# Kernel tuning notes

Measured on AMD Instinct MI355X. Metric: run time of the kernel, lower is better.

## Reference

```python
import jax, jax.numpy as jnp
import numpy as np

N_HEADS = 32
N_KV_HEADS = 8
HEAD_DIM = 64


def _apply_rope(x, cos, sin):
    # x: [b, s, h, d]; cos/sin: [s, d//2]; interleaved real/imag pairs
    xr = x[..., 0::2]
    xi = x[..., 1::2]
    c = cos[None, :, None, :]
    s = sin[None, :, None, :]
    out_r = xr * c - xi * s
    out_i = xr * s + xi * c
    return jnp.stack([out_r, out_i], axis=-1).reshape(x.shape)


def setup_inputs() -> dict:
    key = jax.random.key(0)
    ks = jax.random.split(key, 10)
    b, s, dim = 2, 512, 2048
    cache_len = 1536
    half = HEAD_DIM // 2
    pos = jnp.arange(cache_len, cache_len + s, dtype=jnp.float32)
    inv_freq = 1.0 / (10000.0 ** (jnp.arange(0, half, dtype=jnp.float32) / half))
    ang = pos[:, None] * inv_freq[None, :]
    scale = 0.02
    return {
        "x": jax.random.normal(ks[0], (b, s, dim), jnp.float32),
        "freqs_cos": jnp.cos(ang),
        "freqs_sin": jnp.sin(ang),
        "k_cache": jax.random.normal(ks[1], (b, N_KV_HEADS, cache_len, HEAD_DIM), jnp.float32),
        "v_cache": jax.random.normal(ks[2], (b, N_KV_HEADS, cache_len, HEAD_DIM), jnp.float32),
        "attn_mask": jnp.zeros((s, cache_len + s), jnp.float32),
        "wq": jax.random.normal(ks[3], (N_HEADS * HEAD_DIM, dim), jnp.float32) * scale,
        "wk": jax.random.normal(ks[4], (N_KV_HEADS * HEAD_DIM, dim), jnp.float32) * scale,
        "wv": jax.random.normal(ks[5], (N_KV_HEADS * HEAD_DIM, dim), jnp.float32) * scale,
        "wo": jax.random.normal(ks[6], (dim, N_HEADS * HEAD_DIM), jnp.float32) * scale,
    }


def reference(x, freqs_cos, freqs_sin, k_cache, v_cache, attn_mask, wq, wk, wv, wo):
    b, s, dim = x.shape
    n_rep = N_HEADS // N_KV_HEADS
    # QKV projections (nn.Linear: y = x @ W.T)
    q = (x @ wq.T).reshape(b, s, N_HEADS, HEAD_DIM)
    k = (x @ wk.T).reshape(b, s, N_KV_HEADS, HEAD_DIM)
    v = (x @ wv.T).reshape(b, s, N_KV_HEADS, HEAD_DIM)
    # RoPE on q, k
    q = _apply_rope(q, freqs_cos, freqs_sin)
    k = _apply_rope(k, freqs_cos, freqs_sin)
    # [b, h, s, d]
    q = q.transpose(0, 2, 1, 3)
    k = k.transpose(0, 2, 1, 3)
    v = v.transpose(0, 2, 1, 3)
    new_k, new_v = k, v
    # KV-cache concat along sequence dim
    k_full = jnp.concatenate([k_cache, k], axis=2)
    v_full = jnp.concatenate([v_cache, v], axis=2)
    # GQA: repeat_interleave kv heads
    if n_rep > 1:
        k_full = jnp.repeat(k_full, n_rep, axis=1)
        v_full = jnp.repeat(v_full, n_rep, axis=1)
    # SDPA
    scale = 1.0 / jnp.sqrt(jnp.asarray(HEAD_DIM, x.dtype))
    scores = jnp.einsum("bhqd,bhkd->bhqk", q, k_full) * scale + attn_mask
    probs = jax.nn.softmax(scores, axis=-1)
    out = jnp.einsum("bhqk,bhkd->bhqd", probs, v_full)
    out = out.transpose(0, 2, 1, 3).reshape(b, s, N_HEADS * HEAD_DIM)
    out = out @ wo.T
    return (out, new_k, new_v)
```

## Files before the change

kernel.cpp:

```cpp
#include <hip/hip_runtime.h>

typedef __attribute__((ext_vector_type(8))) short bf16x8;
typedef __attribute__((ext_vector_type(4))) float f32x4;
typedef unsigned short u16;

#define MFMA16(a, b, c) __builtin_amdgcn_mfma_f32_16x16x32_bf16(a, b, c, 0, 0, 0)
#define GLL(srcp, dstp) __builtin_amdgcn_global_load_lds(                      \
    (const __attribute__((address_space(1))) void*)(srcp),                     \
    (__attribute__((address_space(3))) void*)(dstp), 16, 0, 0)

__device__ __forceinline__ u16 f2b(float f) {
  union { float f; unsigned u; } a; a.f = f;
  return (u16)((a.u + 0x7FFFu + ((a.u >> 16) & 1u)) >> 16);
}

__global__ __launch_bounds__(256) void prep(const float* __restrict__ x,
                                            const float* __restrict__ wq,
                                            const float* __restrict__ wk,
                                            const float* __restrict__ wv,
                                            const float* __restrict__ wo,
                                            const float* __restrict__ kc,
                                            u16* __restrict__ xb,
                                            u16* __restrict__ wcat,
                                            u16* __restrict__ wob,
                                            u16* __restrict__ kfull) {
  const int c = blockIdx.x * 256 + threadIdx.x;
  const float* src;
  u16* dst;
  if (c < 524288) {
    src = x + (size_t)c * 4; dst = xb + (size_t)c * 4;
  } else if (c < 1572864) {
    size_t l = c - 524288; src = wq + l * 4; dst = wcat + l * 4;
  } else if (c < 1835008) {
    size_t l = c - 1572864; src = wk + l * 4; dst = wcat + 4194304 + l * 4;
  } else if (c < 2097152) {
    size_t l = c - 1835008; src = wv + l * 4; dst = wcat + 5242880 + l * 4;
  } else if (c < 3145728) {
    size_t l = c - 2097152; src = wo + l * 4; dst = wob + l * 4;
  } else {
    int l = c - 3145728;
    int bh = l / 24576, r = l - bh * 24576;
    src = kc + (size_t)bh * 98304 + (size_t)r * 4;
    dst = kfull + (size_t)bh * 131072 + (size_t)r * 4;
  }
  const float4 v = *(const float4*)src;
  ushort4 o;
  o.x = f2b(v.x); o.y = f2b(v.y); o.z = f2b(v.z); o.w = f2b(v.w);
  *(ushort4*)dst = o;
}

__global__ __launch_bounds__(256) void vtr(const float* __restrict__ vc,
                                           const float* __restrict__ newv,
                                           u16* __restrict__ vT) {
  __shared__ float tile[64][65];
  const int kt = blockIdx.x, bh = blockIdx.y;
  const float* src;
  int colbase;
  if (kt < 24) {
    src = vc + ((size_t)bh * 1536 + (size_t)kt * 64) * 64;
    colbase = kt * 64;
  } else {
    src = newv + ((size_t)bh * 512 + (size_t)(kt - 24) * 64) * 64;
    colbase = 1536 + (kt - 24) * 64;
  }
  const int t = threadIdx.x;
#pragma unroll
  for (int j = 0; j < 4; j++) {
    int e = t + j * 256;
    int r = e >> 4, c = (e & 15) * 4;
    float4 v = *(const float4*)(src + (size_t)r * 64 + c);
    tile[r][c] = v.x; tile[r][c + 1] = v.y; tile[r][c + 2] = v.z; tile[r][c + 3] = v.w;
  }
  __syncthreads();
  int d = t >> 2, kv0 = (t & 3) * 16;
  u16* dst = vT + ((size_t)bh * 64 + d) * 2048 + colbase + kv0;
#pragma unroll
  for (int i = 0; i < 16; i++) dst[i] = f2b(tile[kv0 + i][d]);
}

__global__ __launch_bounds__(256, 1) void gemm_bt(const u16* __restrict__ A,
                                                  const u16* __restrict__ B,
                                                  float* __restrict__ C,
                                                  int M, int N, int K) {
  __shared__ __attribute__((aligned(16))) u16 As[4][8192];
  __shared__ __attribute__((aligned(16))) u16 Bs[4][8192];
  const int t = threadIdx.x;
  const int lane = t & 63, w = t >> 6;
  const int wr = (w >> 1) * 64, wc = (w & 1) * 64;
  const int g = lane >> 4, cc = lane & 15;
  const size_t row0 = (size_t)blockIdx.x * 128, col0 = (size_t)blockIdx.y * 128;

  const int lr = lane >> 3, lc = lane & 7;
  const int swz = lc ^ lr;
  const u16* aS = A + (row0 + w * 32 + lr) * (size_t)K + swz * 8;
  const u16* bS = B + (col0 + w * 32 + lr) * (size_t)K + swz * 8;

  f32x4 acc[4][4] = {};

#define GSTAGE(bufi, kk0)                                                      \
  {                                                                            \
    _Pragma("unroll") for (int i = 0; i < 4; i++) {                            \
      GLL(aS + (size_t)(i * 8) * K + (kk0), &As[bufi][(w * 32 + i * 8) * 64]); \
      GLL(bS + (size_t)(i * 8) * K + (kk0), &Bs[bufi][(w * 32 + i * 8) * 64]); \
    }                                                                          \
  }

  const int niter = K >> 6;
  GSTAGE(0, 0);
  GSTAGE(1, 64);
  GSTAGE(2, 128);
  asm volatile("s_waitcnt vmcnt(16)" ::: "memory");
  __builtin_amdgcn_s_barrier();

  for (int it = 0; it < niter; ++it) {
    const int buf = it & 3;
    if (it + 3 < niter) GSTAGE((it + 3) & 3, (it + 3) * 64);
    bf16x8 av[4][2], bv[4][2];
#pragma unroll
    for (int m = 0; m < 4; m++) {
      const int row = wr + m * 16 + cc;
#pragma unroll
      for (int kk = 0; kk < 2; kk++)
        av[m][kk] = *(const bf16x8*)(&As[buf][row * 64 + (((kk * 4 + g) ^ (cc & 7)) * 8)]);
    }
#pragma unroll
    for (int n = 0; n < 4; n++) {
      const int row = wc + n * 16 + cc;
#pragma unroll
      for (int kk = 0; kk < 2; kk++)
        bv[n][kk] = *(const bf16x8*)(&Bs[buf][row * 64 + (((kk * 4 + g) ^ (cc & 7)) * 8)]);
    }
#pragma unroll
    for (int kk = 0; kk < 2; kk++)
#pragma unroll
      for (int m = 0; m < 4; m++)
#pragma unroll
        for (int n = 0; n < 4; n++)
          acc[m][n] = MFMA16(av[m][kk], bv[n][kk], acc[m][n]);
    if (it + 4 <= niter) {
      asm volatile("s_waitcnt vmcnt(16)" ::: "memory");
    } else if (it + 3 == niter) {
      asm volatile("s_waitcnt vmcnt(8)" ::: "memory");
    } else if (it + 2 == niter) {
      asm volatile("s_waitcnt vmcnt(0)" ::: "memory");
    }
    if (it + 1 < niter) __builtin_amdgcn_s_barrier();
  }
#undef GSTAGE
#pragma unroll
  for (int m = 0; m < 4; m++)
#pragma unroll
    for (int n = 0; n < 4; n++)
#pragma unroll
      for (int r = 0; r < 4; r++)
        C[(row0 + wr + m * 16 + g * 4 + r) * N + (col0 + wc + n * 16 + cc)] = acc[m][n][r];
}

__global__ __launch_bounds__(256) void postproc(const float* __restrict__ Cqkv,
                                                const float* __restrict__ fcos,
                                                const float* __restrict__ fsin,
                                                u16* __restrict__ qrope,
                                                u16* __restrict__ kfull,
                                                float* __restrict__ newk,
                                                float* __restrict__ newv) {
  int idx = blockIdx.x * 256 + threadIdx.x;
  if (idx >= 1024 * 1536) return;
  int m = idx / 1536, p = idx - m * 1536;
  int b = m >> 9, s = m & 511;
  const float* row = Cqkv + (size_t)m * 3072;
  if (p < 1280) {
    bool isq = p < 1024;
    int pk = isq ? p : p - 1024;
    int h = pk >> 5, i = pk & 31;
    int colbase = (isq ? 0 : 2048) + h * 64 + 2 * i;
    float xr = row[colbase], xi = row[colbase + 1];
    float co = fcos[s * 32 + i], si = fsin[s * 32 + i];
    float orr = xr * co - xi * si;
    float oii = xr * si + xi * co;
    if (isq) {
      u16* dst = qrope + (((size_t)(b * 32 + h) * 512 + s) * 64 + 2 * i);
      dst[0] = f2b(orr); dst[1] = f2b(oii);
    } else {
      size_t o0 = ((size_t)(b * 8 + h) * 512 + s) * 64 + 2 * i;
      newk[o0] = orr; newk[o0 + 1] = oii;
      u16* kf = kfull + (((size_t)(b * 8 + h) * 2048 + 1536 + s) * 64 + 2 * i);
      kf[0] = f2b(orr); kf[1] = f2b(oii);
    }
  } else {
    int pv = p - 1280;
    int h = pv >> 5, i = pv & 31;
    float v0 = row[2560 + h * 64 + 2 * i], v1 = row[2560 + h * 64 + 2 * i + 1];
    size_t o0 = ((size_t)(b * 8 + h) * 512 + s) * 64 + 2 * i;
    newv[o0] = v0; newv[o0 + 1] = v1;
  }
}

__global__ __launch_bounds__(512, 4) void attn_split(const u16* __restrict__ qrope,
                                                     const u16* __restrict__ kfull,
                                                     const u16* __restrict__ vT,
                                                     const float* __restrict__ mask,
                                                     float* __restrict__ po,
                                                     float* __restrict__ ml) {
  __shared__ __attribute__((aligned(16))) u16 Ks[4][4096];
  __shared__ __attribute__((aligned(16))) u16 Vs[4][4096];
  __shared__ __attribute__((aligned(16))) u16 P_lds[8192];
  const int t = threadIdx.x, lane = t & 63, w = t >> 6;
  const int g = lane >> 4, cc = lane & 15;
  const int p = blockIdx.x;
  const int v = (p & 7) * 64 + (p >> 3);
  const int bh = v >> 3, qt = (v >> 1) & 3, sp = v & 1;
  const int b = bh >> 5, h = bh & 31;
  const int bhkv = b * 8 + (h >> 2);
  const int s0 = qt * 128 + w * 16;
  const int j0beg = sp * 1024;

  const int lr = lane >> 3, lc = lane & 7;
  const int swzc = lc ^ lr;

  bf16x8 qa0, qa1;
  {
    const u16* qb = qrope + ((size_t)bh * 512 + s0 + cc) * 64 + g * 8;
    qa0 = *(const bf16x8*)qb;
    qa1 = *(const bf16x8*)(qb + 32);
  }
  float mrow[4], lsum[4];
  f32x4 o[4] = {};
#pragma unroll
  for (int r = 0; r < 4; r++) { mrow[r] = -1e30f; lsum[r] = 0.0f; }

  u16* Pw = P_lds + w * 1024;
  const float* mbase = mask + (size_t)(s0 + g * 4) * 2048 + cc;
  const u16* ksrc0 = kfull + (size_t)bhkv * 131072 + (size_t)(w * 8 + lr) * 64 + swzc * 8;
  const u16* vsrc0 = vT + ((size_t)bhkv * 64 + w * 8 + lr) * 2048 + swzc * 8;

#pragma unroll
  for (int pt = 0; pt < 3; ++pt) {
    GLL(ksrc0 + (size_t)(j0beg + pt * 64) * 64, &Ks[pt][w * 512]);
    GLL(vsrc0 + (j0beg + pt * 64), &Vs[pt][w * 512]);
  }

  for (int it = 0; it < 16; ++it) {
    const int buf = it & 3;
    const int j0 = j0beg + it * 64;
    if (it < 14) {
      asm volatile("s_waitcnt vmcnt(4)" ::: "memory");
    } else if (it == 14) {
      asm volatile("s_waitcnt vmcnt(2)" ::: "memory");
    } else {
      asm volatile("s_waitcnt vmcnt(0)" ::: "memory");
    }
    __builtin_amdgcn_s_barrier();

    float mk[4][4];
#pragma unroll
    for (int r = 0; r < 4; r++)
#pragma unroll
      for (int jb = 0; jb < 4; jb++)
        mk[r][jb] = mbase[(size_t)r * 2048 + j0 + jb * 16];
    __builtin_amdgcn_sched_barrier(0);
    if (it < 13) {
      GLL(ksrc0 + (size_t)(j0 + 192) * 64, &Ks[(it + 3) & 3][w * 512]);
      GLL(vsrc0 + (j0 + 192), &Vs[(it + 3) & 3][w * 512]);
    }

    f32x4 sc[4];
    __builtin_amdgcn_s_setprio(1);
#pragma unroll
    for (int jb = 0; jb < 4; jb++) {
      const bf16x8 k0 = *(const bf16x8*)(&Ks[buf][(jb * 16 + cc) * 64 + ((g ^ (cc & 7)) * 8)]);
      const bf16x8 k1 =
          *(const bf16x8*)(&Ks[buf][(jb * 16 + cc) * 64 + (((g + 4) ^ (cc & 7)) * 8)]);
      f32x4 z = {0.f, 0.f, 0.f, 0.f};
      z = MFMA16(qa0, k0, z);
      z = MFMA16(qa1, k1, z);
      sc[jb] = z;
    }
    __builtin_amdgcn_s_setprio(0);
    float pp[4][4];
#pragma unroll
    for (int r = 0; r < 4; r++) {
#pragma unroll
      for (int jb = 0; jb < 4; jb++)
        pp[r][jb] = sc[jb][r] * 0.125f + mk[r][jb];
      const float lm = fmaxf(fmaxf(pp[r][0], pp[r][1]), fmaxf(pp[r][2], pp[r][3]));
      if (__any(lm > mrow[r] + 8.0f)) {
        float tm = lm;
#pragma unroll
        for (int off = 1; off < 16; off <<= 1) tm = fmaxf(tm, __shfl_xor(tm, off, 64));
        const float newm = fmaxf(mrow[r], tm);
        const float corr = __expf(mrow[r] - newm);
        mrow[r] = newm;
        lsum[r] *= corr;
#pragma unroll
        for (int db = 0; db < 4; db++) o[db][r] *= corr;
      }
      float ps = 0.f;
#pragma unroll
      for (int jb = 0; jb < 4; jb++) { pp[r][jb] = __expf(pp[r][jb] - mrow[r]); ps += pp[r][jb]; }
      lsum[r] += ps;
      const int rowb = (g * 4 + r) * 128;
      const int sw = ((g * 4 + r) & 7) << 4;
#pragma unroll
      for (int jb = 0; jb < 4; jb++)
        Pw[((rowb + (jb * 16 + cc) * 2) ^ sw) >> 1] = f2b(pp[r][jb]);
    }
    __builtin_amdgcn_s_setprio(1);
#pragma unroll
    for (int kk = 0; kk < 2; kk++) {
      const bf16x8 pa =
          *(const bf16x8*)(Pw + (((cc * 128 + kk * 64 + g * 16) ^ ((cc & 7) << 4)) >> 1));
#pragma unroll
      for (int db = 0; db < 4; db++) {
        const bf16x8 vf =
            *(const bf16x8*)(&Vs[buf][(db * 16 + cc) * 64 + (((kk * 4 + g) ^ (cc & 7)) * 8)]);
        o[db] = MFMA16(pa, vf, o[db]);
      }
    }
    __builtin_amdgcn_s_setprio(0);
  }
#pragma unroll
  for (int r = 0; r < 4; r++) {
    float ps = lsum[r];
#pragma unroll
    for (int off = 1; off < 16; off <<= 1) ps += __shfl_xor(ps, off, 64);
    const size_t row = (size_t)bh * 512 + s0 + g * 4 + r;
    float* dst = po + (row * 2 + sp) * 64 + cc;
#pragma unroll
    for (int db = 0; db < 4; db++) dst[db * 16] = o[db][r];
    if (cc == 0) {
      float2* mlp = (float2*)ml;
      mlp[row * 2 + sp] = make_float2(mrow[r], ps);
    }
  }
}

__global__ __launch_bounds__(256) void attn_combine(const float* __restrict__ po,
                                                    const float* __restrict__ ml,
                                                    u16* __restrict__ aout) {
  const int t = threadIdx.x;
  const int row = blockIdx.x * 4 + (t >> 6);
  const int d = t & 63;
  const int bh = row >> 9, s = row & 511;
  const int b = bh >> 5, h = bh & 31;
  const float2* mlp = (const float2*)ml;
  const float2 m0 = mlp[row * 2 + 0], m1 = mlp[row * 2 + 1];
  const float M = fmaxf(m0.x, m1.x);
  const float w0 = __expf(m0.x - M), w1 = __expf(m1.x - M);
  const float L = m0.y * w0 + m1.y * w1;
  const float o = po[(size_t)(row * 2 + 0) * 64 + d] * w0 +
                  po[(size_t)(row * 2 + 1) * 64 + d] * w1;
  aout[((size_t)(b * 512 + s)) * 2048 + h * 64 + d] = f2b(o / L);
}

extern "C" void kernel_launch(void* const* d_in, const int* in_sizes, int n_in,
                              void* d_out, int out_size, void* d_ws, size_t ws_size,
                              hipStream_t stream) {
  (void)in_sizes; (void)n_in; (void)out_size; (void)ws_size;
  const float* x    = (const float*)d_in[0];
  const float* fcos = (const float*)d_in[1];
  const float* fsin = (const float*)d_in[2];
  const float* kc   = (const float*)d_in[3];
  const float* vc   = (const float*)d_in[4];
  const float* mask = (const float*)d_in[5];
  const float* wq   = (const float*)d_in[6];
  const float* wk   = (const float*)d_in[7];
  const float* wv   = (const float*)d_in[8];
  const float* wo   = (const float*)d_in[9];

  float* out_f = (float*)d_out;
  float* newk  = out_f + 2097152;
  float* newv  = out_f + 2621440;

  u16*   xb    = (u16*)d_ws;
  u16*   wcat  = xb + 2097152;
  u16*   wob   = wcat + 6291456;
  float* Cqkv  = (float*)(wob + 4194304);
  u16*   qrope = (u16*)(Cqkv + 3145728);
  u16*   kfull = qrope + 2097152;
  u16*   vTf   = kfull + 2097152;
  u16*   aout  = vTf + 2097152;
  float* po    = (float*)d_ws;
  float* ml    = Cqkv;

  prep<<<13824, 256, 0, stream>>>(x, wq, wk, wv, wo, kc, xb, wcat, wob, kfull);

  gemm_bt<<<dim3(8, 24), 256, 0, stream>>>(xb, wcat, Cqkv, 1024, 3072, 2048);
  postproc<<<6144, 256, 0, stream>>>(Cqkv, fcos, fsin, qrope, kfull, newk, newv);
  vtr<<<dim3(32, 16), 256, 0, stream>>>(vc, newv, vTf);
  attn_split<<<512, 512, 0, stream>>>(qrope, kfull, vTf, mask, po, ml);
  attn_combine<<<8192, 256, 0, stream>>>(po, ml, aout);
  gemm_bt<<<dim3(8, 16), 256, 0, stream>>>(aout, wob, out_f, 1024, 2048, 2048);
}
```

Baseline: 147.5 us.

## Fuse fp32 weight-to-bf16 conversion into GEMM B-tile loads

The separate prep pass that converted wq/wk/wv/wo to bf16 in workspace is removed. The GEMM now reads fp32 weights directly through registers, converts them to bf16 and writes them into swizzled LDS. Only the activations still use async global-to-LDS loads. The pipeline drops from a 4-stage async ring to register-staged double buffering, with launch bounds raised to 2 blocks per CU. This avoids a full fp32 read plus bf16 write and re-read of every weight, but each weight element is now converted by all 8 row-blocks and the pipeline is shallower.

```diff
diff --git a/kernel.cpp b/kernel.cpp
--- a/kernel.cpp
+++ b/kernel.cpp
@@ -15,30 +15,16 @@
 }
 
 __global__ __launch_bounds__(256) void prep(const float* __restrict__ x,
-                                            const float* __restrict__ wq,
-                                            const float* __restrict__ wk,
-                                            const float* __restrict__ wv,
-                                            const float* __restrict__ wo,
                                             const float* __restrict__ kc,
                                             u16* __restrict__ xb,
-                                            u16* __restrict__ wcat,
-                                            u16* __restrict__ wob,
                                             u16* __restrict__ kfull) {
   const int c = blockIdx.x * 256 + threadIdx.x;
   const float* src;
   u16* dst;
   if (c < 524288) {
     src = x + (size_t)c * 4; dst = xb + (size_t)c * 4;
-  } else if (c < 1572864) {
-    size_t l = c - 524288; src = wq + l * 4; dst = wcat + l * 4;
-  } else if (c < 1835008) {
-    size_t l = c - 1572864; src = wk + l * 4; dst = wcat + 4194304 + l * 4;
-  } else if (c < 2097152) {
-    size_t l = c - 1835008; src = wv + l * 4; dst = wcat + 5242880 + l * 4;
-  } else if (c < 3145728) {
-    size_t l = c - 2097152; src = wo + l * 4; dst = wob + l * 4;
   } else {
-    int l = c - 3145728;
+    int l = c - 524288;
     int bh = l / 24576, r = l - bh * 24576;
     src = kc + (size_t)bh * 98304 + (size_t)r * 4;
     dst = kfull + (size_t)bh * 131072 + (size_t)r * 4;
@@ -78,43 +64,70 @@
   for (int i = 0; i < 16; i++) dst[i] = f2b(tile[kv0 + i][d]);
 }
 
-__global__ __launch_bounds__(256, 1) void gemm_bt(const u16* __restrict__ A,
-                                                  const u16* __restrict__ B,
+__global__ __launch_bounds__(256, 2) void gemm_bt(const u16* __restrict__ A,
+                                                  const float* __restrict__ B0,
+                                                  const float* __restrict__ B1,
+                                                  const float* __restrict__ B2,
                                                   float* __restrict__ C,
-                                                  int M, int N, int K) {
-  __shared__ __attribute__((aligned(16))) u16 As[4][8192];
-  __shared__ __attribute__((aligned(16))) u16 Bs[4][8192];
+                                                  int M, int N, int K, int nb1, int nb2) {
+  __shared__ __attribute__((aligned(16))) u16 As[2][8192];
+  __shared__ __attribute__((aligned(16))) u16 Bs[2][8192];
   const int t = threadIdx.x;
   const int lane = t & 63, w = t >> 6;
   const int wr = (w >> 1) * 64, wc = (w & 1) * 64;
   const int g = lane >> 4, cc = lane & 15;
-  const size_t row0 = (size_t)blockIdx.x * 128, col0 = (size_t)blockIdx.y * 128;
+  const size_t row0 = (size_t)blockIdx.x * 128;
+  const int col0 = blockIdx.y * 128;
 
   const int lr = lane >> 3, lc = lane & 7;
   const int swz = lc ^ lr;
   const u16* aS = A + (row0 + w * 32 + lr) * (size_t)K + swz * 8;
-  const u16* bS = B + (col0 + w * 32 + lr) * (size_t)K + swz * 8;
+  const float* Bb;
+  int brow;
+  if (col0 < nb1) { Bb = B0; brow = col0; }
+  else if (col0 < nb2) { Bb = B1; brow = col0 - nb1; }
+  else { Bb = B2; brow = col0 - nb2; }
+  const float* bS = Bb + (brow + w * 32 + lr) * (size_t)K + swz * 8;
 
   f32x4 acc[4][4] = {};
-
-#define GSTAGE(bufi, kk0)                                                      \
+  f32x4 bl[4][2];
+
+#define ALOAD(bufi, kk0)                                                       \
+  {                                                                            \
+    _Pragma("unroll") for (int i = 0; i < 4; i++)                              \
+        GLL(aS + (size_t)(i * 8) * K + (kk0), &As[bufi][(w * 32 + i * 8) * 64]); \
+  }
+#define BLOAD(kk0)                                                             \
   {                                                                            \
     _Pragma("unroll") for (int i = 0; i < 4; i++) {                            \
-      GLL(aS + (size_t)(i * 8) * K + (kk0), &As[bufi][(w * 32 + i * 8) * 64]); \
-      GLL(bS + (size_t)(i * 8) * K + (kk0), &Bs[bufi][(w * 32 + i * 8) * 64]); \
+      bl[i][0] = *(const f32x4*)(bS + (size_t)(i * 8) * K + (kk0));            \
+      bl[i][1] = *(const f32x4*)(bS + (size_t)(i * 8) * K + (kk0) + 4);        \
     }                                                                          \
   }
+#define BWRITE(bufi)                                                           \
+  {                                                                            \
+    _Pragma("unroll") for (int i = 0; i < 4; i++) {                            \
+      bf16x8 pk;                                                               \
+      _Pragma("unroll") for (int e = 0; e < 4; e++) {                          \
+        pk[e] = (short)f2b(bl[i][0][e]);                                       \
+        pk[e + 4] = (short)f2b(bl[i][1][e]);                                   \
+      }                                                                        \
+      *(bf16x8*)&Bs[bufi][(w * 32 + i * 8 + lr) * 64 + lc * 8] = pk;           \
+    }                                                                          \
+  }
 
   const int niter = K >> 6;
-  GSTAGE(0, 0);
-  GSTAGE(1, 64);
-  GSTAGE(2, 128);
-  asm volatile("s_waitcnt vmcnt(16)" ::: "memory");
-  __builtin_amdgcn_s_barrier();
+  BLOAD(0);
+  ALOAD(0, 0);
+  BWRITE(0);
+  __syncthreads();
 
   for (int it = 0; it < niter; ++it) {
-    const int buf = it & 3;
-    if (it + 3 < niter) GSTAGE((it + 3) & 3, (it + 3) * 64);
+    const int buf = it & 1;
+    if (it + 1 < niter) {
+      BLOAD((it + 1) * 64);
+      ALOAD(buf ^ 1, (it + 1) * 64);
+    }
     bf16x8 av[4][2], bv[4][2];
 #pragma unroll
     for (int m = 0; m < 4; m++) {
@@ -137,16 +150,12 @@
 #pragma unroll
         for (int n = 0; n < 4; n++)
           acc[m][n] = MFMA16(av[m][kk], bv[n][kk], acc[m][n]);
-    if (it + 4 <= niter) {
-      asm volatile("s_waitcnt vmcnt(16)" ::: "memory");
-    } else if (it + 3 == niter) {
-      asm volatile("s_waitcnt vmcnt(8)" ::: "memory");
-    } else if (it + 2 == niter) {
-      asm volatile("s_waitcnt vmcnt(0)" ::: "memory");
-    }
-    if (it + 1 < niter) __builtin_amdgcn_s_barrier();
-  }
-#undef GSTAGE
+    if (it + 1 < niter) BWRITE(buf ^ 1);
+    __syncthreads();
+  }
+#undef ALOAD
+#undef BLOAD
+#undef BWRITE
 #pragma unroll
   for (int m = 0; m < 4; m++)
 #pragma unroll
@@ -372,22 +381,22 @@
   float* newv  = out_f + 2621440;
 
   u16*   xb    = (u16*)d_ws;
-  u16*   wcat  = xb + 2097152;
-  u16*   wob   = wcat + 6291456;
-  float* Cqkv  = (float*)(wob + 4194304);
+  float* Cqkv  = (float*)(xb + 2097152);
   u16*   qrope = (u16*)(Cqkv + 3145728);
   u16*   kfull = qrope + 2097152;
   u16*   vTf   = kfull + 2097152;
   u16*   aout  = vTf + 2097152;
   float* po    = (float*)d_ws;
-  float* ml    = Cqkv;
-
-  prep<<<13824, 256, 0, stream>>>(x, wq, wk, wv, wo, kc, xb, wcat, wob, kfull);
-
-  gemm_bt<<<dim3(8, 24), 256, 0, stream>>>(xb, wcat, Cqkv, 1024, 3072, 2048);
+  float* ml    = (float*)(aout + 2097152);
+
+  prep<<<3584, 256, 0, stream>>>(x, kc, xb, kfull);
+
+  gemm_bt<<<dim3(8, 24), 256, 0, stream>>>(xb, wq, wk, wv, Cqkv,
+                                           1024, 3072, 2048, 2048, 2560);
   postproc<<<6144, 256, 0, stream>>>(Cqkv, fcos, fsin, qrope, kfull, newk, newv);
   vtr<<<dim3(32, 16), 256, 0, stream>>>(vc, newv, vTf);
   attn_split<<<512, 512, 0, stream>>>(qrope, kfull, vTf, mask, po, ml);
   attn_combine<<<8192, 256, 0, stream>>>(po, ml, aout);
-  gemm_bt<<<dim3(8, 16), 256, 0, stream>>>(aout, wob, out_f, 1024, 2048, 2048);
-}
+  gemm_bt<<<dim3(8, 16), 256, 0, stream>>>(aout, wo, wo, wo, out_f,
+                                           1024, 2048, 2048, 4096, 8192);
+}
```

Result: slower. 180.2 us (+22.1%).
